# Kernel optimization log

Measured on AMD Instinct MI355X. Metric: run time of the kernel, lower is better.

Reference implementation:

```python
import jax, jax.numpy as jnp
import numpy as np

D_MODEL = 512
SEQ_LEN = 2048
S = 32  # local window size
BATCH = 2


def setup_inputs() -> dict:
    key = jax.random.key(0)
    ks = jax.random.split(key, 12)
    shp = (SEQ_LEN, BATCH, D_MODEL)
    return {
        "query": jax.random.normal(ks[0], shp, jnp.float32),
        "key": jax.random.normal(ks[1], shp, jnp.float32),
        "value": jax.random.normal(ks[2], shp, jnp.float32),
        "Wq": jax.random.normal(ks[3], (D_MODEL, D_MODEL), jnp.float32) * 0.02,
        "bq": jax.random.normal(ks[4], (D_MODEL,), jnp.float32) * 0.01,
        "Wk": jax.random.normal(ks[5], (D_MODEL, D_MODEL), jnp.float32) * 0.02,
        "bk": jax.random.normal(ks[6], (D_MODEL,), jnp.float32) * 0.01,
        "Wv": jax.random.normal(ks[7], (D_MODEL, D_MODEL), jnp.float32) * 0.02,
        "bv": jax.random.normal(ks[8], (D_MODEL,), jnp.float32) * 0.01,
        "pos_bias": jax.random.normal(ks[9], (SEQ_LEN, SEQ_LEN), jnp.float32) * 0.02,
        "Wo": jax.random.normal(ks[10], (D_MODEL, D_MODEL), jnp.float32) * 0.02,
        "bo": jax.random.normal(ks[11], (D_MODEL,), jnp.float32) * 0.01,
    }


def _aft_local(query, key, value, Wq, bq, Wk, bk, Wv, bv, pos_bias, Wo, bo):
    T, B, D = query.shape
    q = query @ Wq.T + bq  # [T,B,D]
    k = key @ Wk.T + bk
    v = value @ Wv.T + bv
    pb = pos_bias[:T, :T]

    # max_logit: elementwise max of per-dim key max and (key + col-max of pos_bias) max,
    # then batch index 0 (faithful to original `[0]` indexing) -> shape [D]
    max_logit = jnp.maximum(k.max(axis=0),
                            (k + pb.max(axis=0)[:, None, None]).max(axis=0))[0]

    # out-of-window running sums: tokens t' <= t - S contribute exp(k) (no pos bias)
    ek = jnp.exp(k - max_logit)                 # [T,B,D]
    cs_num = jnp.cumsum(ek * v, axis=0)
    cs_den = jnp.cumsum(ek, axis=0)
    t_arr = jnp.arange(T)
    prefix_idx = jnp.clip(t_arr - S, 0, T - 1)
    has_prefix = (t_arr >= S)[:, None, None]
    num_out = jnp.where(has_prefix, cs_num[prefix_idx], 0.0)
    den_out = jnp.where(has_prefix, cs_den[prefix_idx], 0.0)

    # in-window part: t' in [max(0, t-S+1), t] with pos_bias[t, t']
    j = jnp.arange(S)
    idx_raw = t_arr[:, None] - S + 1 + j[None, :]   # [T,S]
    valid = (idx_raw >= 0).astype(k.dtype)
    idx = jnp.clip(idx_raw, 0, T - 1)
    k_win = k[idx]                                  # [T,S,B,D]
    v_win = v[idx]                                  # [T,S,B,D]
    pb_win = pb[t_arr[:, None], idx]                # [T,S]
    exp_l = jnp.exp(k_win + pb_win[:, :, None, None] - max_logit) * valid[:, :, None, None]
    num_in = (exp_l * v_win).sum(axis=1)            # [T,B,D]
    den_in = exp_l.sum(axis=1)

    y = jax.nn.sigmoid(q) * (num_out + num_in) / (den_out + den_in)
    return y @ Wo.T + bo


def reference(query, key, value, Wq, bq, Wk, bk, Wv, bv, pos_bias, Wo, bo):
    return _aft_local(query, key, value, Wq, bq, Wk, bk, Wv, bv, pos_bias, Wo, bo)
```

## Files before the change

kernel.cpp:

```cpp
#include <hip/hip_runtime.h>
#include <hip/hip_bf16.h>

#define TT 2048
#define BB 2
#define DD 512
#define BD (BB*DD)
#define SS 32
#define MR (TT*BB)
#define NE (TT*BB*DD)
#define CH 32

typedef __bf16 bf16x8 __attribute__((ext_vector_type(8)));
typedef float f32x4 __attribute__((ext_vector_type(4)));

__device__ __forceinline__ void async_copy16(void* lds, const void* gptr) {
    __builtin_amdgcn_global_load_lds(
        (const __attribute__((address_space(1))) void*)gptr,
        (__attribute__((address_space(3))) void*)lds,
        16, 0, 0);
}

__global__ __launch_bounds__(256) void cast_all(
    const float* __restrict__ s0, const float* __restrict__ s1, const float* __restrict__ s2,
    const float* __restrict__ w0, const float* __restrict__ w1,
    const float* __restrict__ w2, const float* __restrict__ w3,
    __hip_bfloat16* __restrict__ d0, __hip_bfloat16* __restrict__ d1, __hip_bfloat16* __restrict__ d2,
    __hip_bfloat16* __restrict__ e0, __hip_bfloat16* __restrict__ e1,
    __hip_bfloat16* __restrict__ e2, __hip_bfloat16* __restrict__ e3)
{
    int b = blockIdx.x;
    const float* s;
    __hip_bfloat16* d;
    size_t i;
    if (b < 6144) {
        int which = b >> 11;
        s = which == 0 ? s0 : (which == 1 ? s1 : s2);
        d = which == 0 ? d0 : (which == 1 ? d1 : d2);
        i = ((size_t)(b & 2047) * 256 + threadIdx.x) * 4;
    } else {
        int b2 = b - 6144;
        int which = b2 >> 8;
        s = which == 0 ? w0 : (which == 1 ? w1 : (which == 2 ? w2 : w3));
        d = which == 0 ? e0 : (which == 1 ? e1 : (which == 2 ? e2 : e3));
        i = ((size_t)(b2 & 255) * 256 + threadIdx.x) * 4;
    }
    float4 f = *(const float4*)(s + i);
    union { __hip_bfloat16 h[4]; ushort4 u; } cv;
    cv.h[0] = __float2bfloat16(f.x); cv.h[1] = __float2bfloat16(f.y);
    cv.h[2] = __float2bfloat16(f.z); cv.h[3] = __float2bfloat16(f.w);
    *(ushort4*)((unsigned short*)d + i) = cv.u;
}

__global__ __launch_bounds__(256) void gemm_qkv(
    const __hip_bfloat16* __restrict__ qb, const __hip_bfloat16* __restrict__ kb,
    const __hip_bfloat16* __restrict__ vb,
    const __hip_bfloat16* __restrict__ Wqb, const __hip_bfloat16* __restrict__ Wkb,
    const __hip_bfloat16* __restrict__ Wvb,
    const float* __restrict__ bq, const float* __restrict__ bk,
    const float* __restrict__ bv,
    float* __restrict__ qout, float* __restrict__ ek, float* __restrict__ ekv,
    float* __restrict__ part_d, float* __restrict__ part_n)
{
    __shared__ char smem[16384];
    const int tid = threadIdx.x;
    const int lane = tid & 63;
    const int wv = tid >> 6;
    const int wave_m = wv >> 1, wave_n = wv & 1;
    const int m0 = blockIdx.y * 64, n0 = blockIdx.x * 64;
    const int kq = lane >> 4, rr = lane & 15;

    if (blockIdx.z == 0) {
        f32x4 acc[2][2] = {};
        const __hip_bfloat16* Arow = qb + (size_t)(m0 + lane) * DD + wv * 8;
        const __hip_bfloat16* Wrow = Wqb + (size_t)(n0 + lane) * DD + wv * 8;
        char* ldsA = &smem[wv * 1024];
        char* ldsW = &smem[4096 + wv * 1024];
        for (int k0 = 0; k0 < DD; k0 += 32) {
            __syncthreads();
            async_copy16(ldsA, Arow + k0);
            async_copy16(ldsW, Wrow + k0);
            __syncthreads();
            bf16x8 a0 = *(const bf16x8*)&smem[kq*1024 + (wave_m*32 +  0 + rr)*16];
            bf16x8 a1 = *(const bf16x8*)&smem[kq*1024 + (wave_m*32 + 16 + rr)*16];
            bf16x8 b0 = *(const bf16x8*)&smem[4096 + kq*1024 + (wave_n*32 +  0 + rr)*16];
            bf16x8 b1 = *(const bf16x8*)&smem[4096 + kq*1024 + (wave_n*32 + 16 + rr)*16];
            acc[0][0] = __builtin_amdgcn_mfma_f32_16x16x32_bf16(a0, b0, acc[0][0], 0, 0, 0);
            acc[0][1] = __builtin_amdgcn_mfma_f32_16x16x32_bf16(a0, b1, acc[0][1], 0, 0, 0);
            acc[1][0] = __builtin_amdgcn_mfma_f32_16x16x32_bf16(a1, b0, acc[1][0], 0, 0, 0);
            acc[1][1] = __builtin_amdgcn_mfma_f32_16x16x32_bf16(a1, b1, acc[1][1], 0, 0, 0);
        }
        #pragma unroll
        for (int ms = 0; ms < 2; ++ms)
            #pragma unroll
            for (int ns = 0; ns < 2; ++ns) {
                int n = n0 + wave_n*32 + ns*16 + rr;
                float bn = bq[n];
                #pragma unroll
                for (int r = 0; r < 4; ++r) {
                    int m = m0 + wave_m*32 + ms*16 + kq*4 + r;
                    qout[(size_t)m * DD + n] = acc[ms][ns][r] + bn;
                }
            }
    } else {
        f32x4 acck[2][2] = {}, accv[2][2] = {};
        const __hip_bfloat16* AKrow = kb + (size_t)(m0 + lane) * DD + wv * 8;
        const __hip_bfloat16* WKrow = Wkb + (size_t)(n0 + lane) * DD + wv * 8;
        const __hip_bfloat16* AVrow = vb + (size_t)(m0 + lane) * DD + wv * 8;
        const __hip_bfloat16* WVrow = Wvb + (size_t)(n0 + lane) * DD + wv * 8;
        char* ldsAK = &smem[wv * 1024];
        char* ldsWK = &smem[4096 + wv * 1024];
        char* ldsAV = &smem[8192 + wv * 1024];
        char* ldsWV = &smem[12288 + wv * 1024];
        for (int k0 = 0; k0 < DD; k0 += 32) {
            __syncthreads();
            async_copy16(ldsAK, AKrow + k0);
            async_copy16(ldsWK, WKrow + k0);
            async_copy16(ldsAV, AVrow + k0);
            async_copy16(ldsWV, WVrow + k0);
            __syncthreads();
            bf16x8 ak0 = *(const bf16x8*)&smem[kq*1024 + (wave_m*32 +  0 + rr)*16];
            bf16x8 ak1 = *(const bf16x8*)&smem[kq*1024 + (wave_m*32 + 16 + rr)*16];
            bf16x8 bk0 = *(const bf16x8*)&smem[4096 + kq*1024 + (wave_n*32 +  0 + rr)*16];
            bf16x8 bk1 = *(const bf16x8*)&smem[4096 + kq*1024 + (wave_n*32 + 16 + rr)*16];
            bf16x8 av0 = *(const bf16x8*)&smem[8192 + kq*1024 + (wave_m*32 +  0 + rr)*16];
            bf16x8 av1 = *(const bf16x8*)&smem[8192 + kq*1024 + (wave_m*32 + 16 + rr)*16];
            bf16x8 bv0 = *(const bf16x8*)&smem[12288 + kq*1024 + (wave_n*32 +  0 + rr)*16];
            bf16x8 bv1 = *(const bf16x8*)&smem[12288 + kq*1024 + (wave_n*32 + 16 + rr)*16];
            acck[0][0] = __builtin_amdgcn_mfma_f32_16x16x32_bf16(ak0, bk0, acck[0][0], 0, 0, 0);
            acck[0][1] = __builtin_amdgcn_mfma_f32_16x16x32_bf16(ak0, bk1, acck[0][1], 0, 0, 0);
            acck[1][0] = __builtin_amdgcn_mfma_f32_16x16x32_bf16(ak1, bk0, acck[1][0], 0, 0, 0);
            acck[1][1] = __builtin_amdgcn_mfma_f32_16x16x32_bf16(ak1, bk1, acck[1][1], 0, 0, 0);
            accv[0][0] = __builtin_amdgcn_mfma_f32_16x16x32_bf16(av0, bv0, accv[0][0], 0, 0, 0);
            accv[0][1] = __builtin_amdgcn_mfma_f32_16x16x32_bf16(av0, bv1, accv[0][1], 0, 0, 0);
            accv[1][0] = __builtin_amdgcn_mfma_f32_16x16x32_bf16(av1, bv0, accv[1][0], 0, 0, 0);
            accv[1][1] = __builtin_amdgcn_mfma_f32_16x16x32_bf16(av1, bv1, accv[1][1], 0, 0, 0);
        }
        float sd[2][2] = {{0.f,0.f},{0.f,0.f}};
        float sn[2][2] = {{0.f,0.f},{0.f,0.f}};
        #pragma unroll
        for (int ms = 0; ms < 2; ++ms)
            #pragma unroll
            for (int ns = 0; ns < 2; ++ns) {
                int n = n0 + wave_n*32 + ns*16 + rr;
                float bkn = bk[n], bvn = bv[n];
                #pragma unroll
                for (int r = 0; r < 4; ++r) {
                    int m = m0 + wave_m*32 + ms*16 + kq*4 + r;
                    float e  = expf(acck[ms][ns][r] + bkn);
                    float nv = e * (accv[ms][ns][r] + bvn);
                    ek[(size_t)m * DD + n]  = e;
                    ekv[(size_t)m * DD + n] = nv;
                    sd[ns][r & 1] += e;
                    sn[ns][r & 1] += nv;
                }
            }
        #pragma unroll
        for (int ns = 0; ns < 2; ++ns)
            #pragma unroll
            for (int par = 0; par < 2; ++par) {
                sd[ns][par] += __shfl_xor(sd[ns][par], 16, 64);
                sd[ns][par] += __shfl_xor(sd[ns][par], 32, 64);
                sn[ns][par] += __shfl_xor(sn[ns][par], 16, 64);
                sn[ns][par] += __shfl_xor(sn[ns][par], 32, 64);
            }
        __syncthreads();
        float* red = (float*)smem;
        if (lane < 16) {
            #pragma unroll
            for (int ns = 0; ns < 2; ++ns) {
                int c = wave_n*32 + ns*16 + rr;
                red[(0*2 + wave_m)*64 + c] = sd[ns][0];
                red[(1*2 + wave_m)*64 + c] = sd[ns][1];
                red[(2*2 + wave_m)*64 + c] = sn[ns][0];
                red[(3*2 + wave_m)*64 + c] = sn[ns][1];
            }
        }
        __syncthreads();
        {
            int which = tid >> 6;
            int c = tid & 63;
            float s = red[(which*2 + 0)*64 + c] + red[(which*2 + 1)*64 + c];
            int b = which & 1;
            float* dst = (which < 2) ? part_d : part_n;
            dst[(size_t)blockIdx.y * BD + b*512 + n0 + c] = s;
        }
    }
}

__global__ __launch_bounds__(256) void fused_window(
    const float* __restrict__ q, const float* __restrict__ ek,
    const float* __restrict__ ekv, const float* __restrict__ part_d,
    const float* __restrict__ part_n, const float* __restrict__ pb,
    __hip_bfloat16* __restrict__ yb)
{
    __shared__ float wl[CH][SS];
    const int tid = threadIdx.x;
    const int col = blockIdx.x * 256 + tid;
    const int chunk = blockIdx.y;
    const int t0 = chunk * CH;

    #pragma unroll
    for (int i = 0; i < (CH * SS) / 256; ++i) {
        int idx = tid + i * 256;
        int tl = idx >> 5, j = idx & 31;
        int t = t0 + tl;
        int u = t - (SS - 1) + j;
        float w = 0.f;
        if (u >= 0) w = expf(pb[(size_t)t * TT + u]);
        wl[tl][j] = w;
    }
    __syncthreads();

    float ring_d[32], ring_n[32];
    float cs_d = 0.f, cs_n = 0.f;
    const bool hasp = (chunk > 0);
    if (hasp) {
        float pref_d = 0.f, pref_n = 0.f;
        for (int p = 0; p < chunk; ++p) {
            pref_d += part_d[(size_t)p * BD + col];
            pref_n += part_n[(size_t)p * BD + col];
        }
        float ssd = 0.f, ssn = 0.f;
        #pragma unroll
        for (int i = 0; i < 32; ++i) {
            size_t off = (size_t)(t0 - 32 + i) * BD + col;
            float e = ek[off];
            float n = ekv[off];
            ring_d[i] = e; ring_n[i] = n;
            ssd += e; ssn += n;
        }
        cs_d = pref_d - ssd;
        cs_n = pref_n - ssn;
    } else {
        #pragma unroll
        for (int i = 0; i < 32; ++i) { ring_d[i] = 0.f; ring_n[i] = 0.f; }
    }

    #pragma unroll
    for (int s = 0; s < CH; ++s) {
        int t = t0 + s;
        size_t off = (size_t)t * BD + col;
        float e = ek[off];
        float n = ekv[off];
        cs_d += ring_d[s];
        cs_n += ring_n[s];
        ring_d[s] = e;
        ring_n[s] = n;
        float den = 0.f, num = 0.f;
        #pragma unroll
        for (int j4 = 0; j4 < 8; ++j4) {
            float4 w4 = *(const float4*)&wl[s][j4 * 4];
            den += w4.x * ring_d[(s + 1 + j4*4 + 0) & 31];
            num += w4.x * ring_n[(s + 1 + j4*4 + 0) & 31];
            den += w4.y * ring_d[(s + 1 + j4*4 + 1) & 31];
            num += w4.y * ring_n[(s + 1 + j4*4 + 1) & 31];
            den += w4.z * ring_d[(s + 1 + j4*4 + 2) & 31];
            num += w4.z * ring_n[(s + 1 + j4*4 + 2) & 31];
            den += w4.w * ring_d[(s + 1 + j4*4 + 3) & 31];
            num += w4.w * ring_n[(s + 1 + j4*4 + 3) & 31];
        }
        if (hasp) { den += cs_d; num += cs_n; }
        float qv = q[off];
        float sig = 1.f / (1.f + expf(-qv));
        yb[off] = __float2bfloat16(sig * num / den);
    }
}

__global__ __launch_bounds__(256) void gemm_out(
    const __hip_bfloat16* __restrict__ yb, const __hip_bfloat16* __restrict__ Wob,
    const float* __restrict__ bo, float* __restrict__ out)
{
    __shared__ char smem[8192];
    const int tid = threadIdx.x;
    const int lane = tid & 63;
    const int wv = tid >> 6;
    const int wave_m = wv >> 1, wave_n = wv & 1;
    const int m0 = blockIdx.y * 64, n0 = blockIdx.x * 64;
    const int kq = lane >> 4, rr = lane & 15;

    f32x4 acc[2][2] = {};
    const __hip_bfloat16* Arow = yb + (size_t)(m0 + lane) * DD + wv * 8;
    const __hip_bfloat16* Wrow = Wob + (size_t)(n0 + lane) * DD + wv * 8;
    char* ldsA = &smem[wv * 1024];
    char* ldsW = &smem[4096 + wv * 1024];

    for (int k0 = 0; k0 < DD; k0 += 32) {
        __syncthreads();
        async_copy16(ldsA, Arow + k0);
        async_copy16(ldsW, Wrow + k0);
        __syncthreads();
        bf16x8 a0 = *(const bf16x8*)&smem[kq*1024 + (wave_m*32 +  0 + rr)*16];
        bf16x8 a1 = *(const bf16x8*)&smem[kq*1024 + (wave_m*32 + 16 + rr)*16];
        bf16x8 b0 = *(const bf16x8*)&smem[4096 + kq*1024 + (wave_n*32 +  0 + rr)*16];
        bf16x8 b1 = *(const bf16x8*)&smem[4096 + kq*1024 + (wave_n*32 + 16 + rr)*16];
        acc[0][0] = __builtin_amdgcn_mfma_f32_16x16x32_bf16(a0, b0, acc[0][0], 0, 0, 0);
        acc[0][1] = __builtin_amdgcn_mfma_f32_16x16x32_bf16(a0, b1, acc[0][1], 0, 0, 0);
        acc[1][0] = __builtin_amdgcn_mfma_f32_16x16x32_bf16(a1, b0, acc[1][0], 0, 0, 0);
        acc[1][1] = __builtin_amdgcn_mfma_f32_16x16x32_bf16(a1, b1, acc[1][1], 0, 0, 0);
    }
    #pragma unroll
    for (int ms = 0; ms < 2; ++ms)
        #pragma unroll
        for (int ns = 0; ns < 2; ++ns) {
            int n = n0 + wave_n*32 + ns*16 + rr;
            float bn = bo[n];
            #pragma unroll
            for (int r = 0; r < 4; ++r) {
                int m = m0 + wave_m*32 + ms*16 + kq*4 + r;
                out[(size_t)m * DD + n] = acc[ms][ns][r] + bn;
            }
        }
}

extern "C" void kernel_launch(void* const* d_in, const int* in_sizes, int n_in,
                              void* d_out, int out_size, void* d_ws, size_t ws_size,
                              hipStream_t stream) {
    const float* query = (const float*)d_in[0];
    const float* key   = (const float*)d_in[1];
    const float* value = (const float*)d_in[2];
    const float* Wq    = (const float*)d_in[3];
    const float* bq    = (const float*)d_in[4];
    const float* Wk    = (const float*)d_in[5];
    const float* bk    = (const float*)d_in[6];
    const float* Wv    = (const float*)d_in[7];
    const float* bv    = (const float*)d_in[8];
    const float* pb    = (const float*)d_in[9];
    const float* Wo    = (const float*)d_in[10];
    const float* bo    = (const float*)d_in[11];
    float* out = (float*)d_out;

    float* ws = (float*)d_ws;
    float* q      = ws;
    float* ek     = ws + (size_t)NE;
    float* ekv    = ws + (size_t)2 * NE;
    float* part_d = ws + (size_t)3 * NE;
    float* part_n = part_d + 65536;
    __hip_bfloat16* bfb = (__hip_bfloat16*)(part_n + 65536);
    __hip_bfloat16* qb  = bfb;
    __hip_bfloat16* kb  = bfb + (size_t)NE;
    __hip_bfloat16* vb  = bfb + (size_t)2 * NE;
    __hip_bfloat16* yb  = bfb + (size_t)3 * NE;
    __hip_bfloat16* Wqb = bfb + (size_t)4 * NE;
    __hip_bfloat16* Wkb = Wqb + 262144;
    __hip_bfloat16* Wvb = Wkb + 262144;
    __hip_bfloat16* Wob = Wvb + 262144;

    cast_all<<<7168, 256, 0, stream>>>(query, key, value, Wq, Wk, Wv, Wo,
                                       qb, kb, vb, Wqb, Wkb, Wvb, Wob);

    gemm_qkv<<<dim3(DD / 64, MR / 64, 2), 256, 0, stream>>>(
        qb, kb, vb, Wqb, Wkb, Wvb, bq, bk, bv,
        q, ek, ekv, part_d, part_n);

    fused_window<<<dim3(BD / 256, TT / CH), 256, 0, stream>>>(
        q, ek, ekv, part_d, part_n, pb, yb);

    gemm_out<<<dim3(DD / 64, MR / 64), 256, 0, stream>>>(yb, Wob, bo, out);
}
```

Baseline: 174.9 us.

## Merge four kernels into one persistent cooperative kernel with grid syncs

Replaces the cast, QKV GEMM, windowed-attention and output GEMM launches with a single cooperative kernel of 512 blocks. The blocks loop over each stage's jobs and separate the stages with grid.sync. This removes launch gaps between kernels but limits parallelism to 512 resident blocks. It also adds grid-wide barrier cost, and the window stage has only 256 jobs, so half the blocks sit idle there.

```diff
diff --git a/kernel.cpp b/kernel.cpp
--- a/kernel.cpp
+++ b/kernel.cpp
@@ -1,5 +1,8 @@
 #include <hip/hip_runtime.h>
 #include <hip/hip_bf16.h>
+#include <hip/hip_cooperative_groups.h>
+
+namespace cg = cooperative_groups;
 
 #define TT 2048
 #define BB 2
@@ -9,6 +12,7 @@
 #define MR (TT*BB)
 #define NE (TT*BB*DD)
 #define CH 32
+#define GRID 512
 
 typedef __bf16 bf16x8 __attribute__((ext_vector_type(8)));
 typedef float f32x4 __attribute__((ext_vector_type(4)));
@@ -20,61 +24,263 @@
         16, 0, 0);
 }
 
-__global__ __launch_bounds__(256) void cast_all(
-    const float* __restrict__ s0, const float* __restrict__ s1, const float* __restrict__ s2,
-    const float* __restrict__ w0, const float* __restrict__ w1,
-    const float* __restrict__ w2, const float* __restrict__ w3,
-    __hip_bfloat16* __restrict__ d0, __hip_bfloat16* __restrict__ d1, __hip_bfloat16* __restrict__ d2,
-    __hip_bfloat16* __restrict__ e0, __hip_bfloat16* __restrict__ e1,
-    __hip_bfloat16* __restrict__ e2, __hip_bfloat16* __restrict__ e3)
-{
-    int b = blockIdx.x;
-    const float* s;
-    __hip_bfloat16* d;
-    size_t i;
-    if (b < 6144) {
-        int which = b >> 11;
-        s = which == 0 ? s0 : (which == 1 ? s1 : s2);
-        d = which == 0 ? d0 : (which == 1 ? d1 : d2);
-        i = ((size_t)(b & 2047) * 256 + threadIdx.x) * 4;
-    } else {
-        int b2 = b - 6144;
-        int which = b2 >> 8;
-        s = which == 0 ? w0 : (which == 1 ? w1 : (which == 2 ? w2 : w3));
-        d = which == 0 ? e0 : (which == 1 ? e1 : (which == 2 ? e2 : e3));
-        i = ((size_t)(b2 & 255) * 256 + threadIdx.x) * 4;
-    }
-    float4 f = *(const float4*)(s + i);
-    union { __hip_bfloat16 h[4]; ushort4 u; } cv;
-    cv.h[0] = __float2bfloat16(f.x); cv.h[1] = __float2bfloat16(f.y);
-    cv.h[2] = __float2bfloat16(f.z); cv.h[3] = __float2bfloat16(f.w);
-    *(ushort4*)((unsigned short*)d + i) = cv.u;
-}
-
-__global__ __launch_bounds__(256) void gemm_qkv(
-    const __hip_bfloat16* __restrict__ qb, const __hip_bfloat16* __restrict__ kb,
-    const __hip_bfloat16* __restrict__ vb,
-    const __hip_bfloat16* __restrict__ Wqb, const __hip_bfloat16* __restrict__ Wkb,
-    const __hip_bfloat16* __restrict__ Wvb,
-    const float* __restrict__ bq, const float* __restrict__ bk,
-    const float* __restrict__ bv,
-    float* __restrict__ qout, float* __restrict__ ek, float* __restrict__ ekv,
-    float* __restrict__ part_d, float* __restrict__ part_n)
+__global__ __launch_bounds__(256, 2) void mega(
+    const float* __restrict__ query, const float* __restrict__ key,
+    const float* __restrict__ value,
+    const float* __restrict__ Wq, const float* __restrict__ bq,
+    const float* __restrict__ Wk, const float* __restrict__ bk,
+    const float* __restrict__ Wv, const float* __restrict__ bv,
+    const float* __restrict__ pb,
+    const float* __restrict__ Wo, const float* __restrict__ bo,
+    float* __restrict__ out,
+    float* __restrict__ q, float* __restrict__ ek, float* __restrict__ ekv,
+    float* __restrict__ part_d, float* __restrict__ part_n,
+    __hip_bfloat16* __restrict__ qb, __hip_bfloat16* __restrict__ kb,
+    __hip_bfloat16* __restrict__ vb, __hip_bfloat16* __restrict__ yb,
+    __hip_bfloat16* __restrict__ Wqb, __hip_bfloat16* __restrict__ Wkb,
+    __hip_bfloat16* __restrict__ Wvb, __hip_bfloat16* __restrict__ Wob)
 {
     __shared__ char smem[16384];
+    cg::grid_group grid = cg::this_grid();
     const int tid = threadIdx.x;
+    const int bid = blockIdx.x;
     const int lane = tid & 63;
-    const int wv = tid >> 6;
-    const int wave_m = wv >> 1, wave_n = wv & 1;
-    const int m0 = blockIdx.y * 64, n0 = blockIdx.x * 64;
+    const int wv_ = tid >> 6;
+    const int wave_m = wv_ >> 1, wave_n = wv_ & 1;
     const int kq = lane >> 4, rr = lane & 15;
 
-    if (blockIdx.z == 0) {
+    for (int b = bid; b < 7168; b += GRID) {
+        const float* s; __hip_bfloat16* d; size_t i;
+        if (b < 6144) {
+            int which = b >> 11;
+            s = which == 0 ? query : (which == 1 ? key : value);
+            d = which == 0 ? qb : (which == 1 ? kb : vb);
+            i = ((size_t)(b & 2047) * 256 + tid) * 4;
+        } else {
+            int b2 = b - 6144;
+            int which = b2 >> 8;
+            s = which == 0 ? Wq : (which == 1 ? Wk : (which == 2 ? Wv : Wo));
+            d = which == 0 ? Wqb : (which == 1 ? Wkb : (which == 2 ? Wvb : Wob));
+            i = ((size_t)(b2 & 255) * 256 + tid) * 4;
+        }
+        float4 f = *(const float4*)(s + i);
+        union { __hip_bfloat16 h[4]; ushort4 u; } cv;
+        cv.h[0] = __float2bfloat16(f.x); cv.h[1] = __float2bfloat16(f.y);
+        cv.h[2] = __float2bfloat16(f.z); cv.h[3] = __float2bfloat16(f.w);
+        *(ushort4*)((unsigned short*)d + i) = cv.u;
+    }
+    grid.sync();
+
+    for (int job = bid; job < 1024; job += GRID) {
+        const int z = job >> 9;
+        const int rem = job & 511;
+        const int n0 = (rem & 7) * 64;
+        const int mt = rem >> 3;
+        const int m0 = mt * 64;
+
+        if (z == 0) {
+            f32x4 acc[2][2] = {};
+            const __hip_bfloat16* Arow = qb + (size_t)(m0 + lane) * DD + wv_ * 8;
+            const __hip_bfloat16* Wrow = Wqb + (size_t)(n0 + lane) * DD + wv_ * 8;
+            char* ldsA = &smem[wv_ * 1024];
+            char* ldsW = &smem[4096 + wv_ * 1024];
+            for (int k0 = 0; k0 < DD; k0 += 32) {
+                __syncthreads();
+                async_copy16(ldsA, Arow + k0);
+                async_copy16(ldsW, Wrow + k0);
+                __syncthreads();
+                bf16x8 a0 = *(const bf16x8*)&smem[kq*1024 + (wave_m*32 +  0 + rr)*16];
+                bf16x8 a1 = *(const bf16x8*)&smem[kq*1024 + (wave_m*32 + 16 + rr)*16];
+                bf16x8 b0 = *(const bf16x8*)&smem[4096 + kq*1024 + (wave_n*32 +  0 + rr)*16];
+                bf16x8 b1 = *(const bf16x8*)&smem[4096 + kq*1024 + (wave_n*32 + 16 + rr)*16];
+                acc[0][0] = __builtin_amdgcn_mfma_f32_16x16x32_bf16(a0, b0, acc[0][0], 0, 0, 0);
+                acc[0][1] = __builtin_amdgcn_mfma_f32_16x16x32_bf16(a0, b1, acc[0][1], 0, 0, 0);
+                acc[1][0] = __builtin_amdgcn_mfma_f32_16x16x32_bf16(a1, b0, acc[1][0], 0, 0, 0);
+                acc[1][1] = __builtin_amdgcn_mfma_f32_16x16x32_bf16(a1, b1, acc[1][1], 0, 0, 0);
+            }
+            #pragma unroll
+            for (int ms = 0; ms < 2; ++ms)
+                #pragma unroll
+                for (int ns = 0; ns < 2; ++ns) {
+                    int n = n0 + wave_n*32 + ns*16 + rr;
+                    float bn = bq[n];
+                    #pragma unroll
+                    for (int r = 0; r < 4; ++r) {
+                        int m = m0 + wave_m*32 + ms*16 + kq*4 + r;
+                        q[(size_t)m * DD + n] = acc[ms][ns][r] + bn;
+                    }
+                }
+            __syncthreads();
+        } else {
+            f32x4 acck[2][2] = {}, accv[2][2] = {};
+            const __hip_bfloat16* AKrow = kb + (size_t)(m0 + lane) * DD + wv_ * 8;
+            const __hip_bfloat16* WKrow = Wkb + (size_t)(n0 + lane) * DD + wv_ * 8;
+            const __hip_bfloat16* AVrow = vb + (size_t)(m0 + lane) * DD + wv_ * 8;
+            const __hip_bfloat16* WVrow = Wvb + (size_t)(n0 + lane) * DD + wv_ * 8;
+            char* ldsAK = &smem[        wv_ * 1024];
+            char* ldsWK = &smem[ 4096 + wv_ * 1024];
+            char* ldsAV = &smem[ 8192 + wv_ * 1024];
+            char* ldsWV = &smem[12288 + wv_ * 1024];
+            for (int k0 = 0; k0 < DD; k0 += 32) {
+                __syncthreads();
+                async_copy16(ldsAK, AKrow + k0);
+                async_copy16(ldsWK, WKrow + k0);
+                async_copy16(ldsAV, AVrow + k0);
+                async_copy16(ldsWV, WVrow + k0);
+                __syncthreads();
+                bf16x8 ak0 = *(const bf16x8*)&smem[kq*1024 + (wave_m*32 +  0 + rr)*16];
+                bf16x8 ak1 = *(const bf16x8*)&smem[kq*1024 + (wave_m*32 + 16 + rr)*16];
+                bf16x8 bk0 = *(const bf16x8*)&smem[4096 + kq*1024 + (wave_n*32 +  0 + rr)*16];
+                bf16x8 bk1 = *(const bf16x8*)&smem[4096 + kq*1024 + (wave_n*32 + 16 + rr)*16];
+                bf16x8 av0 = *(const bf16x8*)&smem[8192 + kq*1024 + (wave_m*32 +  0 + rr)*16];
+                bf16x8 av1 = *(const bf16x8*)&smem[8192 + kq*1024 + (wave_m*32 + 16 + rr)*16];
+                bf16x8 bv0 = *(const bf16x8*)&smem[12288 + kq*1024 + (wave_n*32 +  0 + rr)*16];
+                bf16x8 bv1 = *(const bf16x8*)&smem[12288 + kq*1024 + (wave_n*32 + 16 + rr)*16];
+                acck[0][0] = __builtin_amdgcn_mfma_f32_16x16x32_bf16(ak0, bk0, acck[0][0], 0, 0, 0);
+                acck[0][1] = __builtin_amdgcn_mfma_f32_16x16x32_bf16(ak0, bk1, acck[0][1], 0, 0, 0);
+                acck[1][0] = __builtin_amdgcn_mfma_f32_16x16x32_bf16(ak1, bk0, acck[1][0], 0, 0, 0);
+                acck[1][1] = __builtin_amdgcn_mfma_f32_16x16x32_bf16(ak1, bk1, acck[1][1], 0, 0, 0);
+                accv[0][0] = __builtin_amdgcn_mfma_f32_16x16x32_bf16(av0, bv0, accv[0][0], 0, 0, 0);
+                accv[0][1] = __builtin_amdgcn_mfma_f32_16x16x32_bf16(av0, bv1, accv[0][1], 0, 0, 0);
+                accv[1][0] = __builtin_amdgcn_mfma_f32_16x16x32_bf16(av1, bv0, accv[1][0], 0, 0, 0);
+                accv[1][1] = __builtin_amdgcn_mfma_f32_16x16x32_bf16(av1, bv1, accv[1][1], 0, 0, 0);
+            }
+            float sd[2][2] = {{0.f,0.f},{0.f,0.f}};
+            float sn[2][2] = {{0.f,0.f},{0.f,0.f}};
+            #pragma unroll
+            for (int ms = 0; ms < 2; ++ms)
+                #pragma unroll
+                for (int ns = 0; ns < 2; ++ns) {
+                    int n = n0 + wave_n*32 + ns*16 + rr;
+                    float bkn = bk[n], bvn = bv[n];
+                    #pragma unroll
+                    for (int r = 0; r < 4; ++r) {
+                        int m = m0 + wave_m*32 + ms*16 + kq*4 + r;
+                        float e  = expf(acck[ms][ns][r] + bkn);
+                        float nv = e * (accv[ms][ns][r] + bvn);
+                        ek[(size_t)m * DD + n]  = e;
+                        ekv[(size_t)m * DD + n] = nv;
+                        sd[ns][r & 1] += e;
+                        sn[ns][r & 1] += nv;
+                    }
+                }
+            #pragma unroll
+            for (int ns = 0; ns < 2; ++ns)
+                #pragma unroll
+                for (int par = 0; par < 2; ++par) {
+                    sd[ns][par] += __shfl_xor(sd[ns][par], 16, 64);
+                    sd[ns][par] += __shfl_xor(sd[ns][par], 32, 64);
+                    sn[ns][par] += __shfl_xor(sn[ns][par], 16, 64);
+                    sn[ns][par] += __shfl_xor(sn[ns][par], 32, 64);
+                }
+            __syncthreads();
+            float* red = (float*)smem;
+            if (lane < 16) {
+                #pragma unroll
+                for (int ns = 0; ns < 2; ++ns) {
+                    int c = wave_n*32 + ns*16 + rr;
+                    red[(0*2 + wave_m)*64 + c] = sd[ns][0];
+                    red[(1*2 + wave_m)*64 + c] = sd[ns][1];
+                    red[(2*2 + wave_m)*64 + c] = sn[ns][0];
+                    red[(3*2 + wave_m)*64 + c] = sn[ns][1];
+                }
+            }
+            __syncthreads();
+            {
+                int which = tid >> 6;
+                int c = tid & 63;
+                float s = red[(which*2 + 0)*64 + c] + red[(which*2 + 1)*64 + c];
+                int b = which & 1;
+                float* dst = (which < 2) ? part_d : part_n;
+                dst[(size_t)mt * BD + b*512 + n0 + c] = s;
+            }
+            __syncthreads();
+        }
+    }
+    grid.sync();
+
+    for (int job = bid; job < 256; job += GRID) {
+        float* wl = (float*)smem;
+        const int col = (job & 3) * 256 + tid;
+        const int chunk = job >> 2;
+        const int t0 = chunk * CH;
+
+        #pragma unroll
+        for (int i = 0; i < (CH * SS) / 256; ++i) {
+            int idx = tid + i * 256;
+            int tl = idx >> 5, j = idx & 31;
+            int t = t0 + tl;
+            int u = t - (SS - 1) + j;
+            float w = 0.f;
+            if (u >= 0) w = expf(pb[(size_t)t * TT + u]);
+            wl[tl * SS + j] = w;
+        }
+        __syncthreads();
+
+        float ring_d[32], ring_n[32];
+        float cs_d = 0.f, cs_n = 0.f;
+        const bool hasp = (chunk > 0);
+        if (hasp) {
+            float pref_d = 0.f, pref_n = 0.f;
+            for (int p = 0; p < chunk; ++p) {
+                pref_d += part_d[(size_t)p * BD + col];
+                pref_n += part_n[(size_t)p * BD + col];
+            }
+            float ssd = 0.f, ssn = 0.f;
+            #pragma unroll
+            for (int i = 0; i < 32; ++i) {
+                size_t off = (size_t)(t0 - 32 + i) * BD + col;
+                float e = ek[off];
+                float n = ekv[off];
+                ring_d[i] = e; ring_n[i] = n;
+                ssd += e; ssn += n;
+            }
+            cs_d = pref_d - ssd;
+            cs_n = pref_n - ssn;
+        } else {
+            #pragma unroll
+            for (int i = 0; i < 32; ++i) { ring_d[i] = 0.f; ring_n[i] = 0.f; }
+        }
+
+        #pragma unroll
+        for (int s = 0; s < CH; ++s) {
+            int t = t0 + s;
+            size_t off = (size_t)t * BD + col;
+            float e = ek[off];
+            float n = ekv[off];
+            cs_d += ring_d[s];
+            cs_n += ring_n[s];
+            ring_d[s] = e;
+            ring_n[s] = n;
+            float den = 0.f, num = 0.f;
+            #pragma unroll
+            for (int j4 = 0; j4 < 8; ++j4) {
+                float4 w4 = *(const float4*)&wl[s * SS + j4 * 4];
+                den += w4.x * ring_d[(s + 1 + j4*4 + 0) & 31];
+                num += w4.x * ring_n[(s + 1 + j4*4 + 0) & 31];
+                den += w4.y * ring_d[(s + 1 + j4*4 + 1) & 31];
+                num += w4.y * ring_n[(s + 1 + j4*4 + 1) & 31];
+                den += w4.z * ring_d[(s + 1 + j4*4 + 2) & 31];
+                num += w4.z * ring_n[(s + 1 + j4*4 + 2) & 31];
+                den += w4.w * ring_d[(s + 1 + j4*4 + 3) & 31];
+                num += w4.w * ring_n[(s + 1 + j4*4 + 3) & 31];
+            }
+            if (hasp) { den += cs_d; num += cs_n; }
+            float qv = q[off];
+            float sig = 1.f / (1.f + expf(-qv));
+            yb[off] = __float2bfloat16(sig * num / den);
+        }
+    }
+    grid.sync();
+
+    for (int job = bid; job < 512; job += GRID) {
+        const int n0 = (job & 7) * 64;
+        const int m0 = (job >> 3) * 64;
         f32x4 acc[2][2] = {};
-        const __hip_bfloat16* Arow = qb + (size_t)(m0 + lane) * DD + wv * 8;
-        const __hip_bfloat16* Wrow = Wqb + (size_t)(n0 + lane) * DD + wv * 8;
-        char* ldsA = &smem[wv * 1024];
-        char* ldsW = &smem[4096 + wv * 1024];
+        const __hip_bfloat16* Arow = yb + (size_t)(m0 + lane) * DD + wv_ * 8;
+        const __hip_bfloat16* Wrow = Wob + (size_t)(n0 + lane) * DD + wv_ * 8;
+        char* ldsA = &smem[wv_ * 1024];
+        char* ldsW = &smem[4096 + wv_ * 1024];
         for (int k0 = 0; k0 < DD; k0 += 32) {
             __syncthreads();
             async_copy16(ldsA, Arow + k0);
@@ -94,222 +300,14 @@
             #pragma unroll
             for (int ns = 0; ns < 2; ++ns) {
                 int n = n0 + wave_n*32 + ns*16 + rr;
-                float bn = bq[n];
+                float bn = bo[n];
                 #pragma unroll
                 for (int r = 0; r < 4; ++r) {
                     int m = m0 + wave_m*32 + ms*16 + kq*4 + r;
-                    qout[(size_t)m * DD + n] = acc[ms][ns][r] + bn;
-                }
-            }
-    } else {
-        f32x4 acck[2][2] = {}, accv[2][2] = {};
-        const __hip_bfloat16* AKrow = kb + (size_t)(m0 + lane) * DD + wv * 8;
-        const __hip_bfloat16* WKrow = Wkb + (size_t)(n0 + lane) * DD + wv * 8;
-        const __hip_bfloat16* AVrow = vb + (size_t)(m0 + lane) * DD + wv * 8;
-        const __hip_bfloat16* WVrow = Wvb + (size_t)(n0 + lane) * DD + wv * 8;
-        char* ldsAK = &smem[wv * 1024];
-        char* ldsWK = &smem[4096 + wv * 1024];
-        char* ldsAV = &smem[8192 + wv * 1024];
-        char* ldsWV = &smem[12288 + wv * 1024];
-        for (int k0 = 0; k0 < DD; k0 += 32) {
-            __syncthreads();
-            async_copy16(ldsAK, AKrow + k0);
-            async_copy16(ldsWK, WKrow + k0);
-            async_copy16(ldsAV, AVrow + k0);
-            async_copy16(ldsWV, WVrow + k0);
-            __syncthreads();
-            bf16x8 ak0 = *(const bf16x8*)&smem[kq*1024 + (wave_m*32 +  0 + rr)*16];
-            bf16x8 ak1 = *(const bf16x8*)&smem[kq*1024 + (wave_m*32 + 16 + rr)*16];
-            bf16x8 bk0 = *(const bf16x8*)&smem[4096 + kq*1024 + (wave_n*32 +  0 + rr)*16];
-            bf16x8 bk1 = *(const bf16x8*)&smem[4096 + kq*1024 + (wave_n*32 + 16 + rr)*16];
-            bf16x8 av0 = *(const bf16x8*)&smem[8192 + kq*1024 + (wave_m*32 +  0 + rr)*16];
-            bf16x8 av1 = *(const bf16x8*)&smem[8192 + kq*1024 + (wave_m*32 + 16 + rr)*16];
-            bf16x8 bv0 = *(const bf16x8*)&smem[12288 + kq*1024 + (wave_n*32 +  0 + rr)*16];
-            bf16x8 bv1 = *(const bf16x8*)&smem[12288 + kq*1024 + (wave_n*32 + 16 + rr)*16];
-            acck[0][0] = __builtin_amdgcn_mfma_f32_16x16x32_bf16(ak0, bk0, acck[0][0], 0, 0, 0);
-            acck[0][1] = __builtin_amdgcn_mfma_f32_16x16x32_bf16(ak0, bk1, acck[0][1], 0, 0, 0);
-            acck[1][0] = __builtin_amdgcn_mfma_f32_16x16x32_bf16(ak1, bk0, acck[1][0], 0, 0, 0);
-            acck[1][1] = __builtin_amdgcn_mfma_f32_16x16x32_bf16(ak1, bk1, acck[1][1], 0, 0, 0);
-            accv[0][0] = __builtin_amdgcn_mfma_f32_16x16x32_bf16(av0, bv0, accv[0][0], 0, 0, 0);
-            accv[0][1] = __builtin_amdgcn_mfma_f32_16x16x32_bf16(av0, bv1, accv[0][1], 0, 0, 0);
-            accv[1][0] = __builtin_amdgcn_mfma_f32_16x16x32_bf16(av1, bv0, accv[1][0], 0, 0, 0);
-            accv[1][1] = __builtin_amdgcn_mfma_f32_16x16x32_bf16(av1, bv1, accv[1][1], 0, 0, 0);
-        }
-        float sd[2][2] = {{0.f,0.f},{0.f,0.f}};
-        float sn[2][2] = {{0.f,0.f},{0.f,0.f}};
-        #pragma unroll
-        for (int ms = 0; ms < 2; ++ms)
-            #pragma unroll
-            for (int ns = 0; ns < 2; ++ns) {
-                int n = n0 + wave_n*32 + ns*16 + rr;
-                float bkn = bk[n], bvn = bv[n];
-                #pragma unroll
-                for (int r = 0; r < 4; ++r) {
-                    int m = m0 + wave_m*32 + ms*16 + kq*4 + r;
-                    float e  = expf(acck[ms][ns][r] + bkn);
-                    float nv = e * (accv[ms][ns][r] + bvn);
-                    ek[(size_t)m * DD + n]  = e;
-                    ekv[(size_t)m * DD + n] = nv;
-                    sd[ns][r & 1] += e;
-                    sn[ns][r & 1] += nv;
-                }
-            }
-        #pragma unroll
-        for (int ns = 0; ns < 2; ++ns)
-            #pragma unroll
-            for (int par = 0; par < 2; ++par) {
-                sd[ns][par] += __shfl_xor(sd[ns][par], 16, 64);
-                sd[ns][par] += __shfl_xor(sd[ns][par], 32, 64);
-                sn[ns][par] += __shfl_xor(sn[ns][par], 16, 64);
-                sn[ns][par] += __shfl_xor(sn[ns][par], 32, 64);
-            }
-        __syncthreads();
-        float* red = (float*)smem;
-        if (lane < 16) {
-            #pragma unroll
-            for (int ns = 0; ns < 2; ++ns) {
-                int c = wave_n*32 + ns*16 + rr;
-                red[(0*2 + wave_m)*64 + c] = sd[ns][0];
-                red[(1*2 + wave_m)*64 + c] = sd[ns][1];
-                red[(2*2 + wave_m)*64 + c] = sn[ns][0];
-                red[(3*2 + wave_m)*64 + c] = sn[ns][1];
-            }
-        }
-        __syncthreads();
-        {
-            int which = tid >> 6;
-            int c = tid & 63;
-            float s = red[(which*2 + 0)*64 + c] + red[(which*2 + 1)*64 + c];
-            int b = which & 1;
-            float* dst = (which < 2) ? part_d : part_n;
-            dst[(size_t)blockIdx.y * BD + b*512 + n0 + c] = s;
-        }
+                    out[(size_t)m * DD + n] = acc[ms][ns][r] + bn;
+                }
+            }
     }
-}
-
-__global__ __launch_bounds__(256) void fused_window(
-    const float* __restrict__ q, const float* __restrict__ ek,
-    const float* __restrict__ ekv, const float* __restrict__ part_d,
-    const float* __restrict__ part_n, const float* __restrict__ pb,
-    __hip_bfloat16* __restrict__ yb)
-{
-    __shared__ float wl[CH][SS];
-    const int tid = threadIdx.x;
-    const int col = blockIdx.x * 256 + tid;
-    const int chunk = blockIdx.y;
-    const int t0 = chunk * CH;
-
-    #pragma unroll
-    for (int i = 0; i < (CH * SS) / 256; ++i) {
-        int idx = tid + i * 256;
-        int tl = idx >> 5, j = idx & 31;
-        int t = t0 + tl;
-        int u = t - (SS - 1) + j;
-        float w = 0.f;
-        if (u >= 0) w = expf(pb[(size_t)t * TT + u]);
-        wl[tl][j] = w;
-    }
-    __syncthreads();
-
-    float ring_d[32], ring_n[32];
-    float cs_d = 0.f, cs_n = 0.f;
-    const bool hasp = (chunk > 0);
-    if (hasp) {
-        float pref_d = 0.f, pref_n = 0.f;
-        for (int p = 0; p < chunk; ++p) {
-            pref_d += part_d[(size_t)p * BD + col];
-            pref_n += part_n[(size_t)p * BD + col];
-        }
-        float ssd = 0.f, ssn = 0.f;
-        #pragma unroll
-        for (int i = 0; i < 32; ++i) {
-            size_t off = (size_t)(t0 - 32 + i) * BD + col;
-            float e = ek[off];
-            float n = ekv[off];
-            ring_d[i] = e; ring_n[i] = n;
-            ssd += e; ssn += n;
-        }
-        cs_d = pref_d - ssd;
-        cs_n = pref_n - ssn;
-    } else {
-        #pragma unroll
-        for (int i = 0; i < 32; ++i) { ring_d[i] = 0.f; ring_n[i] = 0.f; }
-    }
-
-    #pragma unroll
-    for (int s = 0; s < CH; ++s) {
-        int t = t0 + s;
-        size_t off = (size_t)t * BD + col;
-        float e = ek[off];
-        float n = ekv[off];
-        cs_d += ring_d[s];
-        cs_n += ring_n[s];
-        ring_d[s] = e;
-        ring_n[s] = n;
-        float den = 0.f, num = 0.f;
-        #pragma unroll
-        for (int j4 = 0; j4 < 8; ++j4) {
-            float4 w4 = *(const float4*)&wl[s][j4 * 4];
-            den += w4.x * ring_d[(s + 1 + j4*4 + 0) & 31];
-            num += w4.x * ring_n[(s + 1 + j4*4 + 0) & 31];
-            den += w4.y * ring_d[(s + 1 + j4*4 + 1) & 31];
-            num += w4.y * ring_n[(s + 1 + j4*4 + 1) & 31];
-            den += w4.z * ring_d[(s + 1 + j4*4 + 2) & 31];
-            num += w4.z * ring_n[(s + 1 + j4*4 + 2) & 31];
-            den += w4.w * ring_d[(s + 1 + j4*4 + 3) & 31];
-            num += w4.w * ring_n[(s + 1 + j4*4 + 3) & 31];
-        }
-        if (hasp) { den += cs_d; num += cs_n; }
-        float qv = q[off];
-        float sig = 1.f / (1.f + expf(-qv));
-        yb[off] = __float2bfloat16(sig * num / den);
-    }
-}
-
-__global__ __launch_bounds__(256) void gemm_out(
-    const __hip_bfloat16* __restrict__ yb, const __hip_bfloat16* __restrict__ Wob,
-    const float* __restrict__ bo, float* __restrict__ out)
-{
-    __shared__ char smem[8192];
-    const int tid = threadIdx.x;
-    const int lane = tid & 63;
-    const int wv = tid >> 6;
-    const int wave_m = wv >> 1, wave_n = wv & 1;
-    const int m0 = blockIdx.y * 64, n0 = blockIdx.x * 64;
-    const int kq = lane >> 4, rr = lane & 15;
-
-    f32x4 acc[2][2] = {};
-    const __hip_bfloat16* Arow = yb + (size_t)(m0 + lane) * DD + wv * 8;
-    const __hip_bfloat16* Wrow = Wob + (size_t)(n0 + lane) * DD + wv * 8;
-    char* ldsA = &smem[wv * 1024];
-    char* ldsW = &smem[4096 + wv * 1024];
-
-    for (int k0 = 0; k0 < DD; k0 += 32) {
-        __syncthreads();
-        async_copy16(ldsA, Arow + k0);
-        async_copy16(ldsW, Wrow + k0);
-        __syncthreads();
-        bf16x8 a0 = *(const bf16x8*)&smem[kq*1024 + (wave_m*32 +  0 + rr)*16];
-        bf16x8 a1 = *(const bf16x8*)&smem[kq*1024 + (wave_m*32 + 16 + rr)*16];
-        bf16x8 b0 = *(const bf16x8*)&smem[4096 + kq*1024 + (wave_n*32 +  0 + rr)*16];
-        bf16x8 b1 = *(const bf16x8*)&smem[4096 + kq*1024 + (wave_n*32 + 16 + rr)*16];
-        acc[0][0] = __builtin_amdgcn_mfma_f32_16x16x32_bf16(a0, b0, acc[0][0], 0, 0, 0);
-        acc[0][1] = __builtin_amdgcn_mfma_f32_16x16x32_bf16(a0, b1, acc[0][1], 0, 0, 0);
-        acc[1][0] = __builtin_amdgcn_mfma_f32_16x16x32_bf16(a1, b0, acc[1][0], 0, 0, 0);
-        acc[1][1] = __builtin_amdgcn_mfma_f32_16x16x32_bf16(a1, b1, acc[1][1], 0, 0, 0);
-    }
-    #pragma unroll
-    for (int ms = 0; ms < 2; ++ms)
-        #pragma unroll
-        for (int ns = 0; ns < 2; ++ns) {
-            int n = n0 + wave_n*32 + ns*16 + rr;
-            float bn = bo[n];
-            #pragma unroll
-            for (int r = 0; r < 4; ++r) {
-                int m = m0 + wave_m*32 + ms*16 + kq*4 + r;
-                out[(size_t)m * DD + n] = acc[ms][ns][r] + bn;
-            }
-        }
 }
 
 extern "C" void kernel_launch(void* const* d_in, const int* in_sizes, int n_in,
@@ -345,15 +343,14 @@
     __hip_bfloat16* Wvb = Wkb + 262144;
     __hip_bfloat16* Wob = Wvb + 262144;
 
-    cast_all<<<7168, 256, 0, stream>>>(query, key, value, Wq, Wk, Wv, Wo,
-                                       qb, kb, vb, Wqb, Wkb, Wvb, Wob);
-
-    gemm_qkv<<<dim3(DD / 64, MR / 64, 2), 256, 0, stream>>>(
-        qb, kb, vb, Wqb, Wkb, Wvb, bq, bk, bv,
-        q, ek, ekv, part_d, part_n);
-
-    fused_window<<<dim3(BD / 256, TT / CH), 256, 0, stream>>>(
-        q, ek, ekv, part_d, part_n, pb, yb);
-
-    gemm_out<<<dim3(DD / 64, MR / 64), 256, 0, stream>>>(yb, Wob, bo, out);
+    void* args[] = {
+        (void*)&query, (void*)&key, (void*)&value,
+        (void*)&Wq, (void*)&bq, (void*)&Wk, (void*)&bk,
+        (void*)&Wv, (void*)&bv, (void*)&pb,
+        (void*)&Wo, (void*)&bo, (void*)&out,
+        (void*)&q, (void*)&ek, (void*)&ekv, (void*)&part_d, (void*)&part_n,
+        (void*)&qb, (void*)&kb, (void*)&vb, (void*)&yb,
+        (void*)&Wqb, (void*)&Wkb, (void*)&Wvb, (void*)&Wob
+    };
+    hipLaunchCooperativeKernel((void*)mega, dim3(GRID), dim3(256), args, 0, stream);
 }
```

After: 379.9 us. 117% more time.
